# Kernel tuning notes

Hardware: AMD Instinct MI355X
Metric: run time of the kernel (lower is better)

## Reference

```python
import jax, jax.numpy as jnp
import numpy as np

B, N, C = 4, 2048, 768
H = 12
DH = C // H
HID = int(C * 4.0)
SCALE = DH ** -0.5
EPS = 1e-5


def layernorm(x, g, b):
    mu = jnp.mean(x, axis=-1, keepdims=True)
    var = jnp.var(x, axis=-1, keepdims=True)
    return (x - mu) * jax.lax.rsqrt(var + EPS) * g + b


def setup_inputs() -> dict:
    key = jax.random.key(0)
    ks = jax.random.split(key, 10)
    s = lambda fan_in: 1.0 / np.sqrt(fan_in)
    return {
        "x": jax.random.normal(ks[0], (B, N, C), dtype=jnp.float32),
        "ln1_g": jnp.ones((C,), jnp.float32),
        "ln1_b": jnp.zeros((C,), jnp.float32),
        "w_qkv": jax.random.uniform(ks[1], (C, 3 * C), jnp.float32, -s(C), s(C)),
        "w_proj": jax.random.uniform(ks[2], (C, C), jnp.float32, -s(C), s(C)),
        "b_proj": jnp.zeros((C,), jnp.float32),
        "ln2_g": jnp.ones((C,), jnp.float32),
        "ln2_b": jnp.zeros((C,), jnp.float32),
        "w_fc1": jax.random.uniform(ks[3], (C, HID), jnp.float32, -s(C), s(C)),
        "b_fc1": jnp.zeros((HID,), jnp.float32),
        "w_fc2": jax.random.uniform(ks[4], (HID, C), jnp.float32, -s(HID), s(HID)),
        "b_fc2": jnp.zeros((C,), jnp.float32),
    }


def reference(x, ln1_g, ln1_b, w_qkv, w_proj, b_proj, ln2_g, ln2_b, w_fc1, b_fc1, w_fc2, b_fc2):
    # --- attention branch ---
    h = layernorm(x, ln1_g, ln1_b)                       # [B,N,C]
    qkv = (h @ w_qkv).reshape(B, N, 3, H, DH)
    q = qkv[:, :, 0].transpose(0, 2, 1, 3)               # [B,H,N,DH]
    k = qkv[:, :, 1].transpose(0, 2, 1, 3)
    v = qkv[:, :, 2].transpose(0, 2, 1, 3)
    attn = jnp.einsum('bhnd,bhmd->bhnm', q, k) * SCALE   # [B,H,N,N]
    attn = jax.nn.softmax(attn, axis=-1)
    y = jnp.einsum('bhnm,bhmd->bhnd', attn, v)           # [B,H,N,DH]
    y = y.transpose(0, 2, 1, 3).reshape(B, N, C)
    y = y @ w_proj + b_proj
    x = x + y
    # --- MLP branch ---
    h = layernorm(x, ln2_g, ln2_b)
    h = jax.nn.gelu(h @ w_fc1 + b_fc1, approximate=False)
    h = h @ w_fc2 + b_fc2
    return x + h
```

## Files before the change

kernel.cpp:

```cpp
#include <hip/hip_runtime.h>
#include <stdint.h>

#define DEV __device__ __forceinline__

typedef __attribute__((ext_vector_type(8))) short bf16x8;
typedef __attribute__((ext_vector_type(4))) float f32x4;
typedef __attribute__((ext_vector_type(4))) short s16x4;

DEV short f2bf(float f) {
    union { float f; unsigned u; } v; v.f = f;
    unsigned r = v.u + 0x7fffu + ((v.u >> 16) & 1u);
    return (short)(r >> 16);
}

DEV uint32_t cvtpk(float lo, float hi) {
    uint32_t r;
    asm("v_cvt_pk_bf16_f32 %0, %1, %2" : "=v"(r) : "v"(lo), "v"(hi));
    return r;
}

typedef const unsigned int __attribute__((address_space(1)))* gp1;
typedef unsigned int __attribute__((address_space(3)))* lp3;

DEV void gload16(const void* g, void* l) {
    __builtin_amdgcn_global_load_lds((gp1)g, (lp3)l, 16, 0, 0);
}

DEV void wait4_barrier() { asm volatile("s_waitcnt vmcnt(4)\ns_barrier" ::: "memory"); }
DEV void wait0_barrier() { asm volatile("s_waitcnt vmcnt(0)\ns_barrier" ::: "memory"); }

__global__ __launch_bounds__(256) void tcvt(
    const float* __restrict__ W, short* __restrict__ WT, int K, int N)
{
    __shared__ float t[32][33];
    int n0 = blockIdx.x * 32, k0 = blockIdx.y * 32;
    int tx = threadIdx.x & 31, ty = threadIdx.x >> 5;
#pragma unroll
    for (int i = 0; i < 32; i += 8)
        t[ty + i][tx] = W[(size_t)(k0 + ty + i) * N + n0 + tx];
    __syncthreads();
#pragma unroll
    for (int i = 0; i < 32; i += 8)
        WT[(size_t)(n0 + ty + i) * K + k0 + tx] = f2bf(t[tx][ty + i]);
}

__global__ __launch_bounds__(256) void ln_bf16(
    const float* __restrict__ x, const float* __restrict__ gam,
    const float* __restrict__ bet, short* __restrict__ out)
{
    const int w = threadIdx.x >> 6, lane = threadIdx.x & 63;
    const size_t row = (size_t)blockIdx.x * 4 + w;
    const float* xr = x + row * 768;
    float4 v[3];
    float s = 0.f, ss = 0.f;
#pragma unroll
    for (int k = 0; k < 3; ++k) {
        v[k] = *(const float4*)(xr + k * 256 + lane * 4);
        s  += v[k].x + v[k].y + v[k].z + v[k].w;
        ss += v[k].x * v[k].x + v[k].y * v[k].y + v[k].z * v[k].z + v[k].w * v[k].w;
    }
#pragma unroll
    for (int i = 1; i < 64; i <<= 1) { s += __shfl_xor(s, i, 64); ss += __shfl_xor(ss, i, 64); }
    const float inv = 1.f / 768.f;
    float mu = s * inv;
    float var = ss * inv - mu * mu;
    float rstd = rsqrtf(var + 1e-5f);
#pragma unroll
    for (int k = 0; k < 3; ++k) {
        int c = k * 256 + lane * 4;
        float vv[4] = { v[k].x, v[k].y, v[k].z, v[k].w };
        s16x4 o;
#pragma unroll
        for (int j = 0; j < 4; ++j)
            o[j] = f2bf((vv[j] - mu) * rstd * gam[c + j] + bet[c + j]);
        *(s16x4*)(out + row * 768 + c) = o;
    }
}

template<int MODE>
__global__ __launch_bounds__(256, 3) void gemm_bf16(
    const short* __restrict__ A, const short* __restrict__ Bt,
    int M, int N, int K,
    const float* __restrict__ bias, const float* __restrict__ resid,
    float* __restrict__ outf, short* __restrict__ outb,
    short* __restrict__ qo, short* __restrict__ ko, short* __restrict__ vo)
{
    __shared__ __align__(16) short As[3][128 * 32];
    __shared__ __align__(16) short Bs[3][128 * 32];
    const int tid = threadIdx.x;
    const int w = tid >> 6, lane = tid & 63;
    const int g = lane >> 4, l15 = lane & 15;
    const int brow = blockIdx.x * 128, bcol = blockIdx.y * 128;
    const int wr = w >> 1, wc = w & 1;
    f32x4 acc[4][4] = {};

    auto stage = [&](int buf, int kt) {
#pragma unroll
        for (int c = 0; c < 2; ++c) {
            int base = w * 2048 + c * 1024;
            int L = base + lane * 16;
            int r = L >> 6;
            int b = L & 63;
            int bs = b ^ ((r & 3) << 4);
            gload16((const char*)(A  + (size_t)(brow + r) * K + kt) + bs, (char*)&As[buf][0] + base);
            gload16((const char*)(Bt + (size_t)(bcol + r) * K + kt) + bs, (char*)&Bs[buf][0] + base);
        }
    };

    const int KT = K >> 5;
    stage(0, 0);
    stage(1, 32);
    wait4_barrier();

    int cur = 0;
    for (int ki = 0; ki < KT; ++ki) {
        if (ki + 2 < KT) {
            int nxt2 = cur + 2; if (nxt2 >= 3) nxt2 -= 3;
            stage(nxt2, (ki + 2) << 5);
        }
        bf16x8 af[4], bfg[4];
#pragma unroll
        for (int m = 0; m < 4; ++m) {
            int r = wr * 64 + m * 16 + l15;
            af[m] = *(const bf16x8*)((const char*)&As[cur][0] + r * 64 + ((g * 16) ^ ((r & 3) << 4)));
        }
#pragma unroll
        for (int n = 0; n < 4; ++n) {
            int r = wc * 64 + n * 16 + l15;
            bfg[n] = *(const bf16x8*)((const char*)&Bs[cur][0] + r * 64 + ((g * 16) ^ ((r & 3) << 4)));
        }
#pragma unroll
        for (int m = 0; m < 4; ++m)
#pragma unroll
            for (int n = 0; n < 4; ++n)
                acc[m][n] = __builtin_amdgcn_mfma_f32_16x16x32_bf16(af[m], bfg[n], acc[m][n], 0, 0, 0);
        if (ki + 1 < KT) {
            if (ki + 2 < KT) wait4_barrier();
            else             wait0_barrier();
        }
        ++cur; if (cur >= 3) cur -= 3;
    }

#pragma unroll
    for (int m = 0; m < 4; ++m) {
#pragma unroll
        for (int n = 0; n < 4; ++n) {
#pragma unroll
            for (int j = 0; j < 4; ++j) {
                int r = brow + wr * 64 + m * 16 + g * 4 + j;
                int c = bcol + wc * 64 + n * 16 + l15;
                float v = acc[m][n][j];
                if (MODE == 0) {
                    int which = c / 768, cc = c % 768;
                    int h = cc >> 6, d = cc & 63;
                    int b_ = r >> 11, nn = r & 2047;
                    size_t bh = (size_t)b_ * 12 + h;
                    if (which == 0)      qo[(bh * 2048 + nn) * 64 + d] = f2bf(v * 0.18033688011112042f);
                    else if (which == 1) ko[(bh * 2048 + nn) * 64 + d] = f2bf(v);
                    else                 vo[(bh * 64 + d) * 2048 + nn] = f2bf(v);
                } else if (MODE == 1) {
                    outf[(size_t)r * N + c] = v + bias[c] + resid[(size_t)r * N + c];
                } else {
                    float t = v + bias[c];
                    float ge = 0.5f * t * (1.0f + erff(t * 0.70710678118654752f));
                    outb[(size_t)r * N + c] = f2bf(ge);
                }
            }
        }
    }
}

__global__ __launch_bounds__(256, 3) void attn_fwd(
    const short* __restrict__ Q, const short* __restrict__ Kg,
    const short* __restrict__ Vt, short* __restrict__ Y)
{
    __shared__ __align__(16) short Kl[2][64 * 64];
    __shared__ __align__(16) short Vl[2][64 * 64];
    __shared__ __align__(16) short Pl[4][32 * 64];
    const int tid = threadIdx.x, w = tid >> 6, lane = tid & 63;
    const int g = lane >> 4, l15 = lane & 15;
    const int bh = blockIdx.y;
    const int q0 = blockIdx.x * 128 + w * 32;
    const short* Qb = Q  + (size_t)bh * 2048 * 64;
    const short* Kb = Kg + (size_t)bh * 2048 * 64;
    const short* Vb = Vt + (size_t)bh * 64 * 2048;

    bf16x8 qf[2][2];
#pragma unroll
    for (int m = 0; m < 2; ++m)
#pragma unroll
        for (int kk = 0; kk < 2; ++kk)
            qf[m][kk] = *(const bf16x8*)(Qb + (size_t)(q0 + m * 16 + l15) * 64 + kk * 32 + g * 8);

    f32x4 accO[2][4] = {};
    float lpart[2] = { 0.f, 0.f };

    auto stage = [&](int buf, int k0) {
#pragma unroll
        for (int c = 0; c < 2; ++c) {
            int bb = w * 2048 + c * 1024;
            int L = bb + lane * 16;
            int r = L >> 7, b = L & 127;
            int bs = b ^ ((r & 7) << 4);
            gload16((const char*)(Kb + (size_t)(k0 + r) * 64) + bs, (char*)(&Kl[buf][0]) + bb);
            gload16((const char*)(Vb + (size_t)r * 2048 + k0) + bs, (char*)(&Vl[buf][0]) + bb);
        }
    };

    stage(0, 0);
    __syncthreads();

    for (int t = 0; t < 32; ++t) {
        const int cur = t & 1;
        if (t < 31) stage(cur ^ 1, (t + 1) * 64);
        const char* Kc = (const char*)&Kl[cur][0];
        const char* Vc = (const char*)&Vl[cur][0];

        f32x4 s[2][4] = {};
        __builtin_amdgcn_s_setprio(1);
#pragma unroll
        for (int kk = 0; kk < 2; ++kk) {
            bf16x8 kf[4];
#pragma unroll
            for (int n = 0; n < 4; ++n) {
                int key = n * 16 + l15;
                kf[n] = *(const bf16x8*)(Kc + key * 128 +
                         (((kk * 32 + g * 8) * 2) ^ ((key & 7) << 4)));
            }
#pragma unroll
            for (int m = 0; m < 2; ++m)
#pragma unroll
                for (int n = 0; n < 4; ++n)
                    s[m][n] = __builtin_amdgcn_mfma_f32_16x16x32_bf16(kf[n], qf[m][kk], s[m][n], 0, 0, 0);
        }
        __builtin_amdgcn_s_setprio(0);

        short* P = &Pl[w][0];
#pragma unroll
        for (int m = 0; m < 2; ++m) {
            int qr = m * 16 + l15;
            char* prow = (char*)P + qr * 128;
            int sw = (qr & 7) << 4;
#pragma unroll
            for (int n = 0; n < 4; ++n) {
                float e0 = __builtin_amdgcn_exp2f(s[m][n][0]);
                float e1 = __builtin_amdgcn_exp2f(s[m][n][1]);
                float e2 = __builtin_amdgcn_exp2f(s[m][n][2]);
                float e3 = __builtin_amdgcn_exp2f(s[m][n][3]);
                lpart[m] += (e0 + e1) + (e2 + e3);
                int keyb = n * 32 + g * 8;
                uint2 pk; pk.x = cvtpk(e0, e1); pk.y = cvtpk(e2, e3);
                *(uint2*)(prow + (keyb ^ sw)) = pk;
            }
        }

        __builtin_amdgcn_s_setprio(1);
#pragma unroll
        for (int kk = 0; kk < 2; ++kk) {
            bf16x8 vf[4], pf[2];
#pragma unroll
            for (int n = 0; n < 4; ++n) {
                int d = n * 16 + l15;
                vf[n] = *(const bf16x8*)(Vc + d * 128 +
                         (((kk * 32 + g * 8) * 2) ^ ((d & 7) << 4)));
            }
#pragma unroll
            for (int m = 0; m < 2; ++m) {
                int qr = m * 16 + l15;
                pf[m] = *(const bf16x8*)((const char*)P + qr * 128 +
                         (((kk * 32 + g * 8) * 2) ^ ((qr & 7) << 4)));
            }
#pragma unroll
            for (int m = 0; m < 2; ++m)
#pragma unroll
                for (int n = 0; n < 4; ++n)
                    accO[m][n] = __builtin_amdgcn_mfma_f32_16x16x32_bf16(pf[m], vf[n], accO[m][n], 0, 0, 0);
        }
        __builtin_amdgcn_s_setprio(0);
        __syncthreads();
    }

#pragma unroll
    for (int m = 0; m < 2; ++m) {
        lpart[m] += __shfl_xor(lpart[m], 16, 64);
        lpart[m] += __shfl_xor(lpart[m], 32, 64);
    }

    int b_ = bh / 12, h = bh % 12;
#pragma unroll
    for (int m = 0; m < 2; ++m) {
        float linv[4];
#pragma unroll
        for (int j = 0; j < 4; ++j)
            linv[j] = 1.0f / __shfl(lpart[m], g * 4 + j, 64);
#pragma unroll
        for (int n = 0; n < 4; ++n)
#pragma unroll
            for (int j = 0; j < 4; ++j) {
                int qq = q0 + m * 16 + g * 4 + j;
                int d = n * 16 + l15;
                Y[((size_t)b_ * 2048 + qq) * 768 + h * 64 + d] = f2bf(accO[m][n][j] * linv[j]);
            }
    }
}

extern "C" void kernel_launch(void* const* d_in, const int* in_sizes, int n_in,
                              void* d_out, int out_size, void* d_ws, size_t ws_size,
                              hipStream_t stream)
{
    const float* x      = (const float*)d_in[0];
    const float* ln1_g  = (const float*)d_in[1];
    const float* ln1_b  = (const float*)d_in[2];
    const float* w_qkv  = (const float*)d_in[3];
    const float* w_proj = (const float*)d_in[4];
    const float* b_proj = (const float*)d_in[5];
    const float* ln2_g  = (const float*)d_in[6];
    const float* ln2_b  = (const float*)d_in[7];
    const float* w_fc1  = (const float*)d_in[8];
    const float* b_fc1  = (const float*)d_in[9];
    const float* w_fc2  = (const float*)d_in[10];
    const float* b_fc2  = (const float*)d_in[11];

    char* ws = (char*)d_ws;
    size_t off = 0;
    auto alloc = [&](size_t bytes) -> void* {
        void* p = ws + off; off += (bytes + 255) & ~(size_t)255; return p;
    };
    short* wqkvT = (short*)alloc((size_t)2304 * 768 * 2);
    short* wprojT= (short*)alloc((size_t)768 * 768 * 2);
    short* wfc1T = (short*)alloc((size_t)3072 * 768 * 2);
    short* wfc2T = (short*)alloc((size_t)768 * 3072 * 2);
    short* h1    = (short*)alloc((size_t)8192 * 768 * 2);
    short* qb    = (short*)alloc((size_t)48 * 2048 * 64 * 2);
    short* kb    = (short*)alloc((size_t)48 * 2048 * 64 * 2);
    short* vtb   = (short*)alloc((size_t)48 * 64 * 2048 * 2);
    short* yb    = (short*)alloc((size_t)8192 * 768 * 2);
    float* X1    = (float*)alloc((size_t)8192 * 768 * 4);
    short* h2    = (short*)alloc((size_t)8192 * 768 * 2);
    short* h3    = (short*)alloc((size_t)8192 * 3072 * 2);

    tcvt<<<dim3(2304 / 32, 768 / 32),  256, 0, stream>>>(w_qkv,  wqkvT,  768,  2304);
    tcvt<<<dim3(768 / 32,  768 / 32),  256, 0, stream>>>(w_proj, wprojT, 768,  768);
    tcvt<<<dim3(3072 / 32, 768 / 32),  256, 0, stream>>>(w_fc1,  wfc1T,  768,  3072);
    tcvt<<<dim3(768 / 32,  3072 / 32), 256, 0, stream>>>(w_fc2,  wfc2T,  3072, 768);

    ln_bf16<<<2048, 256, 0, stream>>>(x, ln1_g, ln1_b, h1);

    gemm_bf16<0><<<dim3(64, 18), 256, 0, stream>>>(h1, wqkvT, 8192, 2304, 768,
        nullptr, nullptr, nullptr, nullptr, qb, kb, vtb);

    attn_fwd<<<dim3(16, 48), 256, 0, stream>>>(qb, kb, vtb, yb);

    gemm_bf16<1><<<dim3(64, 6), 256, 0, stream>>>(yb, wprojT, 8192, 768, 768,
        b_proj, x, X1, nullptr, nullptr, nullptr, nullptr);

    ln_bf16<<<2048, 256, 0, stream>>>(X1, ln2_g, ln2_b, h2);

    gemm_bf16<2><<<dim3(64, 24), 256, 0, stream>>>(h2, wfc1T, 8192, 3072, 768,
        b_fc1, nullptr, nullptr, h3, nullptr, nullptr, nullptr);

    gemm_bf16<1><<<dim3(64, 6), 256, 0, stream>>>(h3, wfc2T, 8192, 768, 3072,
        b_fc2, X1, (float*)d_out, nullptr, nullptr, nullptr, nullptr);
}
```

Baseline: 307.7 us.

## Shrink attention key tiles to 32 with 4-stage pipeline and fix LDS swizzles

The attention kernel now processes 32 keys per iteration with a 4-buffer (3-deep prefetch) LDS ring and vmcnt-based waits instead of a double buffer with full syncthreads. Occupancy is raised to 4 blocks per CU via launch bounds. The LDS XOR swizzle for 64-byte rows in both GEMM and attention switches to ((r>>1)&3) to reduce bank conflicts. The trade-off is more loop iterations with less MFMA work each, so barrier and softmax overhead per key rises.

```diff
diff --git a/kernel.cpp b/kernel.cpp
--- a/kernel.cpp
+++ b/kernel.cpp
@@ -27,6 +27,7 @@
 }
 
 DEV void wait4_barrier() { asm volatile("s_waitcnt vmcnt(4)\ns_barrier" ::: "memory"); }
+DEV void wait2_barrier() { asm volatile("s_waitcnt vmcnt(2)\ns_barrier" ::: "memory"); }
 DEV void wait0_barrier() { asm volatile("s_waitcnt vmcnt(0)\ns_barrier" ::: "memory"); }
 
 __global__ __launch_bounds__(256) void tcvt(
@@ -101,7 +102,7 @@
             int L = base + lane * 16;
             int r = L >> 6;
             int b = L & 63;
-            int bs = b ^ ((r & 3) << 4);
+            int bs = b ^ (((r >> 1) & 3) << 4);
             gload16((const char*)(A  + (size_t)(brow + r) * K + kt) + bs, (char*)&As[buf][0] + base);
             gload16((const char*)(Bt + (size_t)(bcol + r) * K + kt) + bs, (char*)&Bs[buf][0] + base);
         }
@@ -122,12 +123,12 @@
 #pragma unroll
         for (int m = 0; m < 4; ++m) {
             int r = wr * 64 + m * 16 + l15;
-            af[m] = *(const bf16x8*)((const char*)&As[cur][0] + r * 64 + ((g * 16) ^ ((r & 3) << 4)));
+            af[m] = *(const bf16x8*)((const char*)&As[cur][0] + r * 64 + ((g * 16) ^ (((r >> 1) & 3) << 4)));
         }
 #pragma unroll
         for (int n = 0; n < 4; ++n) {
             int r = wc * 64 + n * 16 + l15;
-            bfg[n] = *(const bf16x8*)((const char*)&Bs[cur][0] + r * 64 + ((g * 16) ^ ((r & 3) << 4)));
+            bfg[n] = *(const bf16x8*)((const char*)&Bs[cur][0] + r * 64 + ((g * 16) ^ (((r >> 1) & 3) << 4)));
         }
 #pragma unroll
         for (int m = 0; m < 4; ++m)
@@ -170,13 +171,13 @@
     }
 }
 
-__global__ __launch_bounds__(256, 3) void attn_fwd(
+__global__ __launch_bounds__(256, 4) void attn_fwd(
     const short* __restrict__ Q, const short* __restrict__ Kg,
     const short* __restrict__ Vt, short* __restrict__ Y)
 {
-    __shared__ __align__(16) short Kl[2][64 * 64];
-    __shared__ __align__(16) short Vl[2][64 * 64];
-    __shared__ __align__(16) short Pl[4][32 * 64];
+    __shared__ __align__(16) short Kl[4][32 * 64];
+    __shared__ __align__(16) short Vl[4][64 * 32];
+    __shared__ __align__(16) short Pl[4][32 * 32];
     const int tid = threadIdx.x, w = tid >> 6, lane = tid & 63;
     const int g = lane >> 4, l15 = lane & 15;
     const int bh = blockIdx.y;
@@ -196,41 +197,42 @@
     float lpart[2] = { 0.f, 0.f };
 
     auto stage = [&](int buf, int k0) {
-#pragma unroll
-        for (int c = 0; c < 2; ++c) {
-            int bb = w * 2048 + c * 1024;
-            int L = bb + lane * 16;
-            int r = L >> 7, b = L & 127;
-            int bs = b ^ ((r & 7) << 4);
-            gload16((const char*)(Kb + (size_t)(k0 + r) * 64) + bs, (char*)(&Kl[buf][0]) + bb);
-            gload16((const char*)(Vb + (size_t)r * 2048 + k0) + bs, (char*)(&Vl[buf][0]) + bb);
-        }
+        int bb = w * 1024;
+        int L = bb + lane * 16;
+        int rk = L >> 7, bk_ = L & 127;
+        int bsk = bk_ ^ ((rk & 7) << 4);
+        gload16((const char*)(Kb + (size_t)(k0 + rk) * 64) + bsk, (char*)(&Kl[buf][0]) + bb);
+        int rv = L >> 6, bv = L & 63;
+        int bsv = bv ^ (((rv >> 1) & 3) << 4);
+        gload16((const char*)(Vb + (size_t)rv * 2048 + k0) + bsv, (char*)(&Vl[buf][0]) + bb);
     };
 
     stage(0, 0);
-    __syncthreads();
-
-    for (int t = 0; t < 32; ++t) {
-        const int cur = t & 1;
-        if (t < 31) stage(cur ^ 1, (t + 1) * 64);
+    stage(1, 32);
+    stage(2, 64);
+    wait4_barrier();
+
+    for (int t = 0; t < 64; ++t) {
+        const int cur = t & 3;
+        if (t + 3 < 64) stage((t + 3) & 3, (t + 3) * 32);
         const char* Kc = (const char*)&Kl[cur][0];
         const char* Vc = (const char*)&Vl[cur][0];
 
-        f32x4 s[2][4] = {};
+        f32x4 s[2][2] = {};
         __builtin_amdgcn_s_setprio(1);
 #pragma unroll
         for (int kk = 0; kk < 2; ++kk) {
-            bf16x8 kf[4];
-#pragma unroll
-            for (int n = 0; n < 4; ++n) {
+            bf16x8 kf[2];
+#pragma unroll
+            for (int n = 0; n < 2; ++n) {
                 int key = n * 16 + l15;
                 kf[n] = *(const bf16x8*)(Kc + key * 128 +
-                         (((kk * 32 + g * 8) * 2) ^ ((key & 7) << 4)));
+                         ((kk * 64 + g * 16) ^ ((key & 7) << 4)));
             }
 #pragma unroll
             for (int m = 0; m < 2; ++m)
 #pragma unroll
-                for (int n = 0; n < 4; ++n)
+                for (int n = 0; n < 2; ++n)
                     s[m][n] = __builtin_amdgcn_mfma_f32_16x16x32_bf16(kf[n], qf[m][kk], s[m][n], 0, 0, 0);
         }
         __builtin_amdgcn_s_setprio(0);
@@ -239,10 +241,10 @@
 #pragma unroll
         for (int m = 0; m < 2; ++m) {
             int qr = m * 16 + l15;
-            char* prow = (char*)P + qr * 128;
-            int sw = (qr & 7) << 4;
-#pragma unroll
-            for (int n = 0; n < 4; ++n) {
+            char* prow = (char*)P + qr * 64;
+            int sw = ((qr >> 1) & 3) << 4;
+#pragma unroll
+            for (int n = 0; n < 2; ++n) {
                 float e0 = __builtin_amdgcn_exp2f(s[m][n][0]);
                 float e1 = __builtin_amdgcn_exp2f(s[m][n][1]);
                 float e2 = __builtin_amdgcn_exp2f(s[m][n][2]);
@@ -255,20 +257,17 @@
         }
 
         __builtin_amdgcn_s_setprio(1);
-#pragma unroll
-        for (int kk = 0; kk < 2; ++kk) {
+        {
             bf16x8 vf[4], pf[2];
 #pragma unroll
             for (int n = 0; n < 4; ++n) {
                 int d = n * 16 + l15;
-                vf[n] = *(const bf16x8*)(Vc + d * 128 +
-                         (((kk * 32 + g * 8) * 2) ^ ((d & 7) << 4)));
+                vf[n] = *(const bf16x8*)(Vc + d * 64 + ((g * 16) ^ (((d >> 1) & 3) << 4)));
             }
 #pragma unroll
             for (int m = 0; m < 2; ++m) {
                 int qr = m * 16 + l15;
-                pf[m] = *(const bf16x8*)((const char*)P + qr * 128 +
-                         (((kk * 32 + g * 8) * 2) ^ ((qr & 7) << 4)));
+                pf[m] = *(const bf16x8*)((const char*)P + qr * 64 + ((g * 16) ^ (((qr >> 1) & 3) << 4)));
             }
 #pragma unroll
             for (int m = 0; m < 2; ++m)
@@ -277,7 +276,10 @@
                     accO[m][n] = __builtin_amdgcn_mfma_f32_16x16x32_bf16(pf[m], vf[n], accO[m][n], 0, 0, 0);
         }
         __builtin_amdgcn_s_setprio(0);
-        __syncthreads();
+
+        if (t < 61)      wait4_barrier();
+        else if (t == 61) wait2_barrier();
+        else if (t == 62) wait0_barrier();
     }
 
 #pragma unroll
```

Result: no change. 309.2 us (+0.5%).
